# Kernel optimization log

Measured on AMD Instinct MI355X. Metric: run time of the kernel, lower is better.

## Reference

```python
import jax, jax.numpy as jnp
import numpy as np

ZERO = -1e4  # Semiring.zero (finite log-zero, as in the torch repo)


def semiring_eye(n, dtype=jnp.float32):
    # log-semiring identity: 0 on diagonal, ZERO off-diagonal
    return jnp.where(jnp.eye(n, dtype=bool), jnp.zeros((), dtype), jnp.full((), ZERO, dtype))


def log_bmm(a, b):
    # LogSemiring.bmm: out[..., i, j] = logsumexp_k(a[..., i, k] + b[..., k, j])
    # matmul-based stable form: avoids materializing the [..., i, k, j] tensor
    am = jnp.max(a, axis=-1, keepdims=True)          # [..., i, 1]
    bm = jnp.max(b, axis=-2, keepdims=True)          # [..., 1, j]
    return am + bm + jnp.log(jnp.matmul(jnp.exp(a - am), jnp.exp(b - bm)))


def crf_reduce(potentials):
    # tree-doubling scan, faithful to reduce() in the torch source
    B, L, T, _ = potentials.shape
    n = L.bit_length()
    pad = (1 << n) - L
    eye = jnp.broadcast_to(semiring_eye(T, potentials.dtype), (B, pad, T, T))
    p = jnp.concatenate([potentials, eye], axis=1)
    for _ in range(n):
        p = log_bmm(p[:, 0::2], p[:, 1::2])
    return p[:, 0]  # [B, T, T]


def setup_inputs() -> dict:
    key = jax.random.key(0)
    k1, k2, k3, k4 = jax.random.split(key, 4)
    B, L, T = 32, 1024, 64
    logits = jax.random.normal(k1, (B, L, T), jnp.float32)
    mask = jnp.ones((B, L), dtype=bool)
    # xavier_normal_ for square matrix: std = sqrt(2 / (T + T))
    transitions = jax.random.normal(k2, (T, T), jnp.float32) * np.sqrt(2.0 / (T + T)).astype(np.float32)
    start_states = jax.random.normal(k3, (T,), jnp.float32)
    end_states = jax.random.normal(k4, (T,), jnp.float32)
    return {"logits": logits, "transitions": transitions,
            "start_states": start_states, "end_states": end_states, "mask": mask}


def reference(logits, transitions, start_states, end_states, mask):
    B, L, T = logits.shape
    end_idx = jnp.sum(mask, axis=-1) - 1                      # [B]
    # include_start: add start_states to first step
    logits = logits.at[:, 0].add(start_states)
    # include_end: scatter-add end_states at last unmasked step
    logits = logits.at[jnp.arange(B), end_idx].add(end_states)
    # zero out padded positions
    logits = logits * mask[..., None]
    me = mask[:, 1:, None, None]                              # [B, L-1, 1, 1]
    trans = transitions[None, None] * me                      # [B, L-1, T, T]
    # LogSemiring.mul == add
    pot = logits[:, 1:, None, :] + trans                      # [B, L-1, T, T]
    pot = pot * me + semiring_eye(T, logits.dtype) * (~me)
    red = crf_reduce(pot)                                     # [B, T, T]
    red = red + logits[:, 0][..., None]                       # start_potentials[..., None]
    return jax.nn.logsumexp(red, axis=(-1, -2))               # [B] log-partition
```

## Files before the change

kernel.cpp:

```cpp
#include <hip/hip_runtime.h>
#include <hip/hip_bf16.h>

typedef __attribute__((ext_vector_type(8))) short short8;
typedef __attribute__((ext_vector_type(4))) float floatx4;
typedef __attribute__((ext_vector_type(4))) unsigned int uint4v;
typedef __attribute__((ext_vector_type(2))) unsigned int uint2v;

#define L_SEQ    1024
#define N_BATCH  32
#define CHUNKA   64
#define NCHUNKA  16
#define REC_SH   4096
#define MST      72

__device__ __forceinline__ unsigned short f2bf(float f) {
    unsigned u = __builtin_bit_cast(unsigned, f);
    return (unsigned short)((u + 0x8000u) >> 16);
}
__device__ __forceinline__ float bf2f(unsigned short h) {
    return __builtin_bit_cast(float, ((unsigned)h) << 16);
}
__device__ __forceinline__ unsigned pkbf(float hi, float lo) {
    unsigned uh = __builtin_bit_cast(unsigned, hi) + 0x8000u;
    unsigned ul = __builtin_bit_cast(unsigned, lo) + 0x8000u;
    return __builtin_amdgcn_perm(uh, ul, 0x07060302u);
}

__device__ __forceinline__ void gload_lds16(const void* g, void* l) {
    __builtin_amdgcn_global_load_lds(
        (const __attribute__((address_space(1))) void*)g,
        (__attribute__((address_space(3))) void*)l, 16, 0, 0);
}

__device__ __forceinline__ int rec_idx(int n, int u) {
    return n * 64 + (u ^ (n & 7)) * 8;
}

__device__ __forceinline__ short8 ldA(const unsigned short* rec, int n, int h, int q) {
    const int u0 = 4 * h + (q >> 1), sub = (q & 1) * 4;
    uint2v lo = *(const uint2v*)(rec + n * 64 + ((u0 ^ (n & 7)) * 8) + sub);
    uint2v hi = *(const uint2v*)(rec + n * 64 + (((u0 + 2) ^ (n & 7)) * 8) + sub);
    uint4v r = {lo[0], lo[1], hi[0], hi[1]};
    return __builtin_bit_cast(short8, r);
}

#define MFMA16(A, B, C) __builtin_amdgcn_mfma_f32_16x16x32_bf16((A), (B), (C), 0, 0, 0)

__global__ __launch_bounds__(256, 4) void crf_phaseA(
    const float* __restrict__ logits, const float* __restrict__ trans,
    const float* __restrict__ end_states, unsigned short* __restrict__ wsA,
    float* __restrict__ sclA)
{
    __shared__ __align__(16) unsigned short Me[64 * MST];
    __shared__ __align__(16) float LdsE[CHUNKA * 64];
    __shared__ float offs[4];

    const int tid = threadIdx.x, lane = tid & 63, w = tid >> 6;
    const int q = lane >> 4, c = lane & 15, R0 = w * 16;
    const int b = blockIdx.y, chunk = blockIdx.x;

    const int l0 = 1 + chunk * CHUNKA;
    const int isTail = (chunk == NCHUNKA - 1);
    const int stageBase = l0 - (isTail ? 1 : 0);
    const int nsteps = isTail ? (L_SEQ - l0) : CHUNKA;

    {
        const float* gsrc = logits + (size_t)b * L_SEQ * 64 + (size_t)stageBase * 64;
        #pragma unroll
        for (int i = 0; i < 4; ++i) {
            const int ch = 4 * w + i;
            gload_lds16(gsrc + ch * 256 + lane * 4, &LdsE[ch * 256]);
        }
    }

    short8 bfr[4][2];
    #pragma unroll
    for (int t = 0; t < 4; ++t) {
        #pragma unroll
        for (int h = 0; h < 2; ++h) {
            short8 v;
            #pragma unroll
            for (int j = 0; j < 8; ++j) {
                const int kk = (2 * h + (j >> 2)) * 16 + q * 4 + (j & 3);
                v[j] = (short)f2bf(__expf(trans[kk * 64 + t * 16 + c]));
            }
            bfr[t][h] = v;
        }
    }
    __syncthreads();

    for (int i = tid; i < CHUNKA * 64 / 4; i += 256) {
        floatx4 v = ((floatx4*)LdsE)[i];
        if (stageBase + (i >> 4) == L_SEQ - 1) {
            const int j0 = (i & 15) * 4;
            #pragma unroll
            for (int e = 0; e < 4; ++e) v[e] += end_states[j0 + e];
        }
        #pragma unroll
        for (int e = 0; e < 4; ++e) v[e] = __expf(v[e]);
        ((floatx4*)LdsE)[i] = v;
    }
    __syncthreads();

    unsigned P[8];
    #pragma unroll
    for (int t = 0; t < 4; ++t) {
        float h0 = (t * 16 + q * 4 + 0 == R0 + c) ? 1.f : 0.f;
        float h1 = (t * 16 + q * 4 + 1 == R0 + c) ? 1.f : 0.f;
        float h2 = (t * 16 + q * 4 + 2 == R0 + c) ? 1.f : 0.f;
        float h3 = (t * 16 + q * 4 + 3 == R0 + c) ? 1.f : 0.f;
        P[2 * t]     = pkbf(h1, h0);
        P[2 * t + 1] = pkbf(h3, h2);
    }

    float off = 0.f;

    auto stepf = [&](int li, bool renorm) {
        floatx4 ewv[4];
        #pragma unroll
        for (int t = 0; t < 4; ++t)
            ewv[t] = *(const floatx4*)&LdsE[li * 64 + t * 16 + q * 4];

        const short8 b0 = __builtin_bit_cast(short8, (uint4v){P[0], P[1], P[2], P[3]});
        const short8 b1 = __builtin_bit_cast(short8, (uint4v){P[4], P[5], P[6], P[7]});

        float h[4][4];
        #pragma unroll
        for (int t = 0; t < 4; ++t) {
            floatx4 z = {0.f, 0.f, 0.f, 0.f};
            z = MFMA16(bfr[t][0], b0, z);
            z = MFMA16(bfr[t][1], b1, z);
            #pragma unroll
            for (int r = 0; r < 4; ++r) h[t][r] = z[r] * ewv[t][r];
        }

        if (renorm) {
            float m = h[0][0];
            #pragma unroll
            for (int t = 0; t < 4; ++t)
                #pragma unroll
                for (int r = 0; r < 4; ++r) m = fmaxf(m, h[t][r]);
            #pragma unroll
            for (int d = 32; d >= 1; d >>= 1) m = fmaxf(m, __shfl_xor(m, d, 64));
            m = fmaxf(m, 1e-30f);
            float inv = __builtin_amdgcn_rcpf(m);
            off += __logf(m);
            #pragma unroll
            for (int t = 0; t < 4; ++t)
                #pragma unroll
                for (int r = 0; r < 4; ++r) h[t][r] *= inv;
        }

        #pragma unroll
        for (int t = 0; t < 4; ++t) {
            P[2 * t]     = pkbf(h[t][1], h[t][0]);
            P[2 * t + 1] = pkbf(h[t][3], h[t][2]);
        }
    };

    const int liBase = l0 - stageBase;
    if (!isTail) {
        for (int g = 0; g < CHUNKA / 8; ++g) {
            #pragma unroll
            for (int k = 0; k < 8; ++k)
                stepf(liBase + g * 8 + k, k == 7);
        }
    } else {
        for (int s = 0; s < nsteps; ++s)
            stepf(liBase + s, ((s & 7) == 7) || (s == nsteps - 1));
    }

    {
        unsigned short* wrow = &Me[(R0 + c) * MST];
        #pragma unroll
        for (int t = 0; t < 4; ++t) {
            uint2v d = {P[2 * t], P[2 * t + 1]};
            *(uint2v*)(wrow + t * 16 + q * 4) = d;
        }
    }
    if (lane == 0) offs[w] = off;
    __syncthreads();

    float omax = fmaxf(fmaxf(offs[0], offs[1]), fmaxf(offs[2], offs[3]));
    const int rid = b * NCHUNKA + chunk;
    unsigned short* rec = wsA + (size_t)rid * REC_SH;
    const int n = tid & 63, qq = tid >> 6;
    float eo = __expf(offs[qq] - omax);
    unsigned short tmp[16] __attribute__((aligned(16)));
    #pragma unroll
    for (int r = 0; r < 16; ++r)
        tmp[r] = f2bf(bf2f(Me[(qq * 16 + r) * MST + n]) * eo);
    *(uint4v*)(rec + rec_idx(n, 2 * qq))     = *(uint4v*)(tmp);
    *(uint4v*)(rec + rec_idx(n, 2 * qq + 1)) = *(uint4v*)(tmp + 8);
    if (tid == 0) sclA[rid] = omax;
}

template<int NSTEPS>
__global__ __launch_bounds__(512) void crf_final(
    const unsigned short* __restrict__ inRecs, const float* __restrict__ sclIn,
    const float* __restrict__ logits, const float* __restrict__ start_states,
    float* __restrict__ out)
{
    __shared__ __align__(16) unsigned short stage[NSTEPS][REC_SH];
    __shared__ __align__(16) unsigned short Me[64 * MST];
    __shared__ float offs[4];
    __shared__ float offsB[4];
    __shared__ float es[64];
    __shared__ float redA;
    __shared__ float wsum[4];

    const int tid = threadIdx.x, lane = tid & 63, w = tid >> 6;
    const int q = lane >> 4, c = lane & 15;
    const int wq = w & 3, chain = w >> 2, R0 = wq * 16;
    const int b = blockIdx.y;
    const int recBase = b * NSTEPS;
    constexpr int HALF = NSTEPS / 2;

    #pragma unroll
    for (int r = 0; r < NSTEPS; ++r) {
        const unsigned short* src = inRecs + (size_t)(recBase + r) * REC_SH;
        gload_lds16(src + w * 512 + lane * 8, &stage[r][w * 512]);
    }

    float sstep[HALF];
    #pragma unroll
    for (int s = 0; s < HALF; ++s)
        sstep[s] = sclIn[recBase + chain * HALF + s];

    unsigned P[8];
    #pragma unroll
    for (int t = 0; t < 4; ++t) {
        float h0 = (t * 16 + q * 4 + 0 == R0 + c) ? 1.f : 0.f;
        float h1 = (t * 16 + q * 4 + 1 == R0 + c) ? 1.f : 0.f;
        float h2 = (t * 16 + q * 4 + 2 == R0 + c) ? 1.f : 0.f;
        float h3 = (t * 16 + q * 4 + 3 == R0 + c) ? 1.f : 0.f;
        P[2 * t]     = pkbf(h1, h0);
        P[2 * t + 1] = pkbf(h3, h2);
    }

    __syncthreads();

    float off = 0.f;
    #pragma unroll
    for (int s = 0; s < HALF; ++s) {
        const unsigned short* rec = stage[chain * HALF + s];
        off += sstep[s];

        const short8 b0 = __builtin_bit_cast(short8, (uint4v){P[0], P[1], P[2], P[3]});
        const short8 b1 = __builtin_bit_cast(short8, (uint4v){P[4], P[5], P[6], P[7]});

        float h[4][4];
        #pragma unroll
        for (int t = 0; t < 4; ++t) {
            const int n = t * 16 + c;
            short8 a0 = ldA(rec, n, 0, q);
            short8 a1 = ldA(rec, n, 1, q);
            floatx4 z = {0.f, 0.f, 0.f, 0.f};
            z = MFMA16(a0, b0, z);
            z = MFMA16(a1, b1, z);
            #pragma unroll
            for (int r = 0; r < 4; ++r) h[t][r] = z[r];
        }

        #pragma unroll
        for (int t = 0; t < 4; ++t) {
            P[2 * t]     = pkbf(h[t][1], h[t][0]);
            P[2 * t + 1] = pkbf(h[t][3], h[t][2]);
        }
    }

    if (chain == 1) {
        unsigned short* wrow = &Me[(R0 + c) * MST];
        #pragma unroll
        for (int t = 0; t < 4; ++t) {
            uint2v d = {P[2 * t], P[2 * t + 1]};
            *(uint2v*)(wrow + t * 16 + q * 4) = d;
        }
        if (lane == 0) offsB[wq] = off;
    }
    __syncthreads();

    unsigned short* PBrec = stage[0];
    const float omaxB = fmaxf(fmaxf(offsB[0], offsB[1]), fmaxf(offsB[2], offsB[3]));
    if (tid < 256) {
        const int n = tid & 63, qq = tid >> 6;
        const float eoB = __expf(offsB[qq] - omaxB);
        unsigned short tmp[16] __attribute__((aligned(16)));
        #pragma unroll
        for (int r = 0; r < 16; ++r)
            tmp[r] = f2bf(bf2f(Me[(qq * 16 + r) * MST + n]) * eoB);
        *(uint4v*)(PBrec + rec_idx(n, 2 * qq))     = *(uint4v*)(tmp);
        *(uint4v*)(PBrec + rec_idx(n, 2 * qq + 1)) = *(uint4v*)(tmp + 8);
    }
    __syncthreads();

    if (chain == 0) {
        off += omaxB;
        const short8 b0 = __builtin_bit_cast(short8, (uint4v){P[0], P[1], P[2], P[3]});
        const short8 b1 = __builtin_bit_cast(short8, (uint4v){P[4], P[5], P[6], P[7]});
        float h[4][4];
        #pragma unroll
        for (int t = 0; t < 4; ++t) {
            const int n = t * 16 + c;
            short8 a0 = ldA(PBrec, n, 0, q);
            short8 a1 = ldA(PBrec, n, 1, q);
            floatx4 z = {0.f, 0.f, 0.f, 0.f};
            z = MFMA16(a0, b0, z);
            z = MFMA16(a1, b1, z);
            #pragma unroll
            for (int r = 0; r < 4; ++r) h[t][r] = z[r];
        }

        {
            float m = h[0][0];
            #pragma unroll
            for (int t = 0; t < 4; ++t)
                #pragma unroll
                for (int r = 0; r < 4; ++r) m = fmaxf(m, h[t][r]);
            #pragma unroll
            for (int d = 32; d >= 1; d >>= 1) m = fmaxf(m, __shfl_xor(m, d, 64));
            m = fmaxf(m, 1e-30f);
            float inv = __builtin_amdgcn_rcpf(m);
            off += __logf(m);
            #pragma unroll
            for (int t = 0; t < 4; ++t)
                #pragma unroll
                for (int r = 0; r < 4; ++r) h[t][r] *= inv;
        }

        #pragma unroll
        for (int t = 0; t < 4; ++t) {
            P[2 * t]     = pkbf(h[t][1], h[t][0]);
            P[2 * t + 1] = pkbf(h[t][3], h[t][2]);
        }

        unsigned short* wrow = &Me[(R0 + c) * MST];
        #pragma unroll
        for (int t = 0; t < 4; ++t) {
            uint2v d = {P[2 * t], P[2 * t + 1]};
            *(uint2v*)(wrow + t * 16 + q * 4) = d;
        }
        if (lane == 0) offs[wq] = off;
    }
    __syncthreads();

    if (w == 0) {
        float u = offs[lane >> 4] + logits[(size_t)b * L_SEQ * 64 + lane]
                  + start_states[lane];
        float A1 = u;
        #pragma unroll
        for (int d = 32; d >= 1; d >>= 1) A1 = fmaxf(A1, __shfl_xor(A1, d, 64));
        es[lane] = __expf(u - A1);
        if (lane == 0) redA = A1;
    }
    __syncthreads();
    if (tid < 256) {
        const int i = tid >> 2, jb = (tid & 3) * 16;
        float sum = 0.f;
        #pragma unroll
        for (int j = 0; j < 16; ++j) sum += bf2f(Me[i * MST + jb + j]);
        sum *= es[i];
        #pragma unroll
        for (int d = 32; d >= 1; d >>= 1) sum += __shfl_xor(sum, d, 64);
        if (lane == 0) wsum[w] = sum;
    }
    __syncthreads();
    if (tid == 0)
        out[b] = redA + __logf(wsum[0] + wsum[1] + wsum[2] + wsum[3]);
}

extern "C" void kernel_launch(void* const* d_in, const int* in_sizes, int n_in,
                              void* d_out, int out_size, void* d_ws, size_t ws_size,
                              hipStream_t stream)
{
    const float* logits       = (const float*)d_in[0];
    const float* trans        = (const float*)d_in[1];
    const float* start_states = (const float*)d_in[2];
    const float* end_states   = (const float*)d_in[3];

    unsigned short* wsA = (unsigned short*)d_ws;
    float* sclA = (float*)(wsA + (size_t)N_BATCH * NCHUNKA * REC_SH);
    float* out  = (float*)d_out;

    crf_phaseA<<<dim3(NCHUNKA, N_BATCH), 256, 0, stream>>>(
        logits, trans, end_states, wsA, sclA);
    crf_final<NCHUNKA><<<dim3(1, N_BATCH), 512, 0, stream>>>(
        wsA, sclA, logits, start_states, out);
}
```

Before: 94.63 us.

## Split phase-A chunk scan into two parallel chains, serialize final combine

Phase A now runs 512 threads per block: two groups of four waves each scan half of the 64-step chunk in parallel, and the two partial products are then combined with one extra MFMA matrix product through shared memory. In exchange, the final kernel drops its two-chain split and runs all 16 chunk records in one serial chain with 256 threads, renormalising only once at step 7. The aim is to shorten the sequential dependency chain in the dominant phase-A kernel. The cost is a longer serial chain in the small final kernel, plus extra LDS and a 512-thread launch bound in phase A that may reduce occupancy.

```diff
diff --git a/kernel.cpp b/kernel.cpp
--- a/kernel.cpp
+++ b/kernel.cpp
@@ -46,17 +46,20 @@
 
 #define MFMA16(A, B, C) __builtin_amdgcn_mfma_f32_16x16x32_bf16((A), (B), (C), 0, 0, 0)
 
-__global__ __launch_bounds__(256, 4) void crf_phaseA(
+__global__ __launch_bounds__(512, 4) void crf_phaseA(
     const float* __restrict__ logits, const float* __restrict__ trans,
     const float* __restrict__ end_states, unsigned short* __restrict__ wsA,
     float* __restrict__ sclA)
 {
     __shared__ __align__(16) unsigned short Me[64 * MST];
     __shared__ __align__(16) float LdsE[CHUNKA * 64];
+    __shared__ __align__(16) unsigned short PBrec[REC_SH];
     __shared__ float offs[4];
+    __shared__ float offsB[4];
 
     const int tid = threadIdx.x, lane = tid & 63, w = tid >> 6;
-    const int q = lane >> 4, c = lane & 15, R0 = w * 16;
+    const int q = lane >> 4, c = lane & 15;
+    const int wq = w & 3, chain = w >> 2, R0 = wq * 16;
     const int b = blockIdx.y, chunk = blockIdx.x;
 
     const int l0 = 1 + chunk * CHUNKA;
@@ -67,8 +70,8 @@
     {
         const float* gsrc = logits + (size_t)b * L_SEQ * 64 + (size_t)stageBase * 64;
         #pragma unroll
-        for (int i = 0; i < 4; ++i) {
-            const int ch = 4 * w + i;
+        for (int i = 0; i < 2; ++i) {
+            const int ch = 2 * w + i;
             gload_lds16(gsrc + ch * 256 + lane * 4, &LdsE[ch * 256]);
         }
     }
@@ -89,7 +92,7 @@
     }
     __syncthreads();
 
-    for (int i = tid; i < CHUNKA * 64 / 4; i += 256) {
+    for (int i = tid; i < CHUNKA * 64 / 4; i += 512) {
         floatx4 v = ((floatx4*)LdsE)[i];
         if (stageBase + (i >> 4) == L_SEQ - 1) {
             const int j0 = (i & 15) * 4;
@@ -159,44 +162,111 @@
     };
 
     const int liBase = l0 - stageBase;
+    const int base = chain * 32;
     if (!isTail) {
-        for (int g = 0; g < CHUNKA / 8; ++g) {
+        for (int g = 0; g < 4; ++g) {
             #pragma unroll
             for (int k = 0; k < 8; ++k)
-                stepf(liBase + g * 8 + k, k == 7);
+                stepf(liBase + base + g * 8 + k, k == 7);
         }
     } else {
-        for (int s = 0; s < nsteps; ++s)
-            stepf(liBase + s, ((s & 7) == 7) || (s == nsteps - 1));
-    }
-
-    {
+        const int count = chain ? 31 : 32;
+        for (int s = 0; s < count; ++s)
+            stepf(liBase + base + s, ((s & 7) == 7) || (s == count - 1));
+    }
+
+    if (chain == 1) {
         unsigned short* wrow = &Me[(R0 + c) * MST];
         #pragma unroll
         for (int t = 0; t < 4; ++t) {
             uint2v d = {P[2 * t], P[2 * t + 1]};
             *(uint2v*)(wrow + t * 16 + q * 4) = d;
         }
-    }
-    if (lane == 0) offs[w] = off;
-    __syncthreads();
-
-    float omax = fmaxf(fmaxf(offs[0], offs[1]), fmaxf(offs[2], offs[3]));
-    const int rid = b * NCHUNKA + chunk;
-    unsigned short* rec = wsA + (size_t)rid * REC_SH;
-    const int n = tid & 63, qq = tid >> 6;
-    float eo = __expf(offs[qq] - omax);
-    unsigned short tmp[16] __attribute__((aligned(16)));
-    #pragma unroll
-    for (int r = 0; r < 16; ++r)
-        tmp[r] = f2bf(bf2f(Me[(qq * 16 + r) * MST + n]) * eo);
-    *(uint4v*)(rec + rec_idx(n, 2 * qq))     = *(uint4v*)(tmp);
-    *(uint4v*)(rec + rec_idx(n, 2 * qq + 1)) = *(uint4v*)(tmp + 8);
-    if (tid == 0) sclA[rid] = omax;
+        if (lane == 0) offsB[wq] = off;
+    }
+    __syncthreads();
+
+    const float omaxB = fmaxf(fmaxf(offsB[0], offsB[1]), fmaxf(offsB[2], offsB[3]));
+    if (tid < 256) {
+        const int n = tid & 63, qq = tid >> 6;
+        const float eoB = __expf(offsB[qq] - omaxB);
+        unsigned short tmp[16] __attribute__((aligned(16)));
+        #pragma unroll
+        for (int r = 0; r < 16; ++r)
+            tmp[r] = f2bf(bf2f(Me[(qq * 16 + r) * MST + n]) * eoB);
+        *(uint4v*)(PBrec + rec_idx(n, 2 * qq))     = *(uint4v*)(tmp);
+        *(uint4v*)(PBrec + rec_idx(n, 2 * qq + 1)) = *(uint4v*)(tmp + 8);
+    }
+    __syncthreads();
+
+    if (chain == 0) {
+        off += omaxB;
+        const short8 b0 = __builtin_bit_cast(short8, (uint4v){P[0], P[1], P[2], P[3]});
+        const short8 b1 = __builtin_bit_cast(short8, (uint4v){P[4], P[5], P[6], P[7]});
+        float h[4][4];
+        #pragma unroll
+        for (int t = 0; t < 4; ++t) {
+            const int n = t * 16 + c;
+            short8 a0 = ldA(PBrec, n, 0, q);
+            short8 a1 = ldA(PBrec, n, 1, q);
+            floatx4 z = {0.f, 0.f, 0.f, 0.f};
+            z = MFMA16(a0, b0, z);
+            z = MFMA16(a1, b1, z);
+            #pragma unroll
+            for (int r = 0; r < 4; ++r) h[t][r] = z[r];
+        }
+
+        {
+            float m = h[0][0];
+            #pragma unroll
+            for (int t = 0; t < 4; ++t)
+                #pragma unroll
+                for (int r = 0; r < 4; ++r) m = fmaxf(m, h[t][r]);
+            #pragma unroll
+            for (int d = 32; d >= 1; d >>= 1) m = fmaxf(m, __shfl_xor(m, d, 64));
+            m = fmaxf(m, 1e-30f);
+            float inv = __builtin_amdgcn_rcpf(m);
+            off += __logf(m);
+            #pragma unroll
+            for (int t = 0; t < 4; ++t)
+                #pragma unroll
+                for (int r = 0; r < 4; ++r) h[t][r] *= inv;
+        }
+
+        #pragma unroll
+        for (int t = 0; t < 4; ++t) {
+            P[2 * t]     = pkbf(h[t][1], h[t][0]);
+            P[2 * t + 1] = pkbf(h[t][3], h[t][2]);
+        }
+
+        unsigned short* wrow = &Me[(R0 + c) * MST];
+        #pragma unroll
+        for (int t = 0; t < 4; ++t) {
+            uint2v d = {P[2 * t], P[2 * t + 1]};
+            *(uint2v*)(wrow + t * 16 + q * 4) = d;
+        }
+        if (lane == 0) offs[wq] = off;
+    }
+    __syncthreads();
+
+    if (tid < 256) {
+        const float omax = fmaxf(fmaxf(offs[0], offs[1]), fmaxf(offs[2], offs[3]));
+        const int rid = b * NCHUNKA + chunk;
+        unsigned short* rec = wsA + (size_t)rid * REC_SH;
+        const int n = tid & 63, qq = tid >> 6;
+        float eo = __expf(offs[qq] - omax);
+        unsigned short tmp[16] __attribute__((aligned(16)));
+        #pragma unroll
+        for (int r = 0; r < 16; ++r)
+            tmp[r] = f2bf(bf2f(Me[(qq * 16 + r) * MST + n]) * eo);
+        *(uint4v*)(rec + rec_idx(n, 2 * qq))     = *(uint4v*)(tmp);
+        *(uint4v*)(rec + rec_idx(n, 2 * qq + 1)) = *(uint4v*)(tmp + 8);
+        if (tid == 0) sclA[rid] = omax;
+    }
 }
 
 template<int NSTEPS>
-__global__ __launch_bounds__(512) void crf_final(
+__global__ __launch_bounds__(256) void crf_final(
     const unsigned short* __restrict__ inRecs, const float* __restrict__ sclIn,
     const float* __restrict__ logits, const float* __restrict__ start_states,
     float* __restrict__ out)
@@ -204,28 +274,28 @@
     __shared__ __align__(16) unsigned short stage[NSTEPS][REC_SH];
     __shared__ __align__(16) unsigned short Me[64 * MST];
     __shared__ float offs[4];
-    __shared__ float offsB[4];
     __shared__ float es[64];
     __shared__ float redA;
     __shared__ float wsum[4];
 
     const int tid = threadIdx.x, lane = tid & 63, w = tid >> 6;
-    const int q = lane >> 4, c = lane & 15;
-    const int wq = w & 3, chain = w >> 2, R0 = wq * 16;
+    const int q = lane >> 4, c = lane & 15, R0 = w * 16;
     const int b = blockIdx.y;
     const int recBase = b * NSTEPS;
-    constexpr int HALF = NSTEPS / 2;
 
     #pragma unroll
     for (int r = 0; r < NSTEPS; ++r) {
         const unsigned short* src = inRecs + (size_t)(recBase + r) * REC_SH;
-        gload_lds16(src + w * 512 + lane * 8, &stage[r][w * 512]);
-    }
-
-    float sstep[HALF];
-    #pragma unroll
-    for (int s = 0; s < HALF; ++s)
-        sstep[s] = sclIn[recBase + chain * HALF + s];
+        #pragma unroll
+        for (int i = 0; i < 2; ++i) {
+            const int ch = 2 * w + i;
+            gload_lds16(src + ch * 512 + lane * 8, &stage[r][ch * 512]);
+        }
+    }
+
+    float sstep[NSTEPS];
+    #pragma unroll
+    for (int s = 0; s < NSTEPS; ++s) sstep[s] = sclIn[recBase + s];
 
     unsigned P[8];
     #pragma unroll
@@ -242,8 +312,8 @@
 
     float off = 0.f;
     #pragma unroll
-    for (int s = 0; s < HALF; ++s) {
-        const unsigned short* rec = stage[chain * HALF + s];
+    for (int s = 0; s < NSTEPS; ++s) {
+        const unsigned short* rec = stage[s];
         off += sstep[s];
 
         const short8 b0 = __builtin_bit_cast(short8, (uint4v){P[0], P[1], P[2], P[3]});
@@ -262,56 +332,7 @@
             for (int r = 0; r < 4; ++r) h[t][r] = z[r];
         }
 
-        #pragma unroll
-        for (int t = 0; t < 4; ++t) {
-            P[2 * t]     = pkbf(h[t][1], h[t][0]);
-            P[2 * t + 1] = pkbf(h[t][3], h[t][2]);
-        }
-    }
-
-    if (chain == 1) {
-        unsigned short* wrow = &Me[(R0 + c) * MST];
-        #pragma unroll
-        for (int t = 0; t < 4; ++t) {
-            uint2v d = {P[2 * t], P[2 * t + 1]};
-            *(uint2v*)(wrow + t * 16 + q * 4) = d;
-        }
-        if (lane == 0) offsB[wq] = off;
-    }
-    __syncthreads();
-
-    unsigned short* PBrec = stage[0];
-    const float omaxB = fmaxf(fmaxf(offsB[0], offsB[1]), fmaxf(offsB[2], offsB[3]));
-    if (tid < 256) {
-        const int n = tid & 63, qq = tid >> 6;
-        const float eoB = __expf(offsB[qq] - omaxB);
-        unsigned short tmp[16] __attribute__((aligned(16)));
-        #pragma unroll
-        for (int r = 0; r < 16; ++r)
-            tmp[r] = f2bf(bf2f(Me[(qq * 16 + r) * MST + n]) * eoB);
-        *(uint4v*)(PBrec + rec_idx(n, 2 * qq))     = *(uint4v*)(tmp);
-        *(uint4v*)(PBrec + rec_idx(n, 2 * qq + 1)) = *(uint4v*)(tmp + 8);
-    }
-    __syncthreads();
-
-    if (chain == 0) {
-        off += omaxB;
-        const short8 b0 = __builtin_bit_cast(short8, (uint4v){P[0], P[1], P[2], P[3]});
-        const short8 b1 = __builtin_bit_cast(short8, (uint4v){P[4], P[5], P[6], P[7]});
-        float h[4][4];
-        #pragma unroll
-        for (int t = 0; t < 4; ++t) {
-            const int n = t * 16 + c;
-            short8 a0 = ldA(PBrec, n, 0, q);
-            short8 a1 = ldA(PBrec, n, 1, q);
-            floatx4 z = {0.f, 0.f, 0.f, 0.f};
-            z = MFMA16(a0, b0, z);
-            z = MFMA16(a1, b1, z);
-            #pragma unroll
-            for (int r = 0; r < 4; ++r) h[t][r] = z[r];
-        }
-
-        {
+        if (s == 7) {
             float m = h[0][0];
             #pragma unroll
             for (int t = 0; t < 4; ++t)
@@ -333,15 +354,17 @@
             P[2 * t]     = pkbf(h[t][1], h[t][0]);
             P[2 * t + 1] = pkbf(h[t][3], h[t][2]);
         }
-
+    }
+
+    {
         unsigned short* wrow = &Me[(R0 + c) * MST];
         #pragma unroll
         for (int t = 0; t < 4; ++t) {
             uint2v d = {P[2 * t], P[2 * t + 1]};
             *(uint2v*)(wrow + t * 16 + q * 4) = d;
         }
-        if (lane == 0) offs[wq] = off;
-    }
+    }
+    if (lane == 0) offs[w] = off;
     __syncthreads();
 
     if (w == 0) {
@@ -354,16 +377,14 @@
         if (lane == 0) redA = A1;
     }
     __syncthreads();
-    if (tid < 256) {
-        const int i = tid >> 2, jb = (tid & 3) * 16;
-        float sum = 0.f;
-        #pragma unroll
-        for (int j = 0; j < 16; ++j) sum += bf2f(Me[i * MST + jb + j]);
-        sum *= es[i];
-        #pragma unroll
-        for (int d = 32; d >= 1; d >>= 1) sum += __shfl_xor(sum, d, 64);
-        if (lane == 0) wsum[w] = sum;
-    }
+    const int i = tid >> 2, jb = (tid & 3) * 16;
+    float sum = 0.f;
+    #pragma unroll
+    for (int j = 0; j < 16; ++j) sum += bf2f(Me[i * MST + jb + j]);
+    sum *= es[i];
+    #pragma unroll
+    for (int d = 32; d >= 1; d >>= 1) sum += __shfl_xor(sum, d, 64);
+    if (lane == 0) wsum[w] = sum;
     __syncthreads();
     if (tid == 0)
         out[b] = redA + __logf(wsum[0] + wsum[1] + wsum[2] + wsum[3]);
@@ -382,8 +403,8 @@
     float* sclA = (float*)(wsA + (size_t)N_BATCH * NCHUNKA * REC_SH);
     float* out  = (float*)d_out;
 
-    crf_phaseA<<<dim3(NCHUNKA, N_BATCH), 256, 0, stream>>>(
+    crf_phaseA<<<dim3(NCHUNKA, N_BATCH), 512, 0, stream>>>(
         logits, trans, end_states, wsA, sclA);
-    crf_final<NCHUNKA><<<dim3(1, N_BATCH), 512, 0, stream>>>(
+    crf_final<NCHUNKA><<<dim3(1, N_BATCH), 256, 0, stream>>>(
         wsA, sclA, logits, start_states, out);
 }
```

Result: no change. 95.30 us (+0.7%).
